# Kernel optimization log

Hardware: AMD Instinct MI355X
Metric: run time of the kernel (lower is better)

## Reference

```python
import math
import jax, jax.numpy as jnp
import numpy as np

B, S, D, H, REL_V = 2, 2048, 1024, 16, 64
HD = D // H
EPS = 1e-5


def _layernorm(x, w, b):
    # torch-style: std with Bessel correction (unbiased), divide by (std + eps)
    u = x.mean(-1, keepdims=True)
    xc = x - u
    s = jnp.sqrt((xc * xc).sum(-1, keepdims=True) / (x.shape[-1] - 1))
    return w * (xc / (s + EPS)) + b


def _gelu(x):
    return 0.5 * x * (1 + jnp.tanh(math.sqrt(2 / math.pi) * (x + 0.044715 * x ** 3)))


def setup_inputs() -> dict:
    key = jax.random.key(0)
    ks = jax.random.split(key, 6)
    wscale = 0.02
    return {
        "x": jax.random.normal(ks[0], (B, S, D), jnp.float32),
        "rel": jax.random.randint(ks[1], (B, S, S), 0, REL_V, jnp.int32),
        "ln1_w": jnp.ones((D,), jnp.float32),
        "ln1_b": jnp.zeros((D,), jnp.float32),
        "Wqkv": jax.random.normal(ks[2], (D, 3 * D), jnp.float32) * wscale,
        "bqkv": jnp.zeros((3 * D,), jnp.float32),
        "Wo": jax.random.normal(ks[3], (D, D), jnp.float32) * wscale,
        "bo": jnp.zeros((D,), jnp.float32),
        "rel_emb": jax.random.normal(ks[4], (REL_V, H), jnp.float32) * wscale,
        "ln2_w": jnp.ones((D,), jnp.float32),
        "ln2_b": jnp.zeros((D,), jnp.float32),
        "Wfc": jax.random.normal(ks[5], (D, 4 * D), jnp.float32) * wscale,
        "bfc": jnp.zeros((4 * D,), jnp.float32),
        "Wp": jax.random.normal(jax.random.fold_in(key, 7), (4 * D, D), jnp.float32) * wscale,
        "bp": jnp.zeros((D,), jnp.float32),
    }


def reference(x, rel, ln1_w, ln1_b, Wqkv, bqkv, Wo, bo, rel_emb,
              ln2_w, ln2_b, Wfc, bfc, Wp, bp):
    h = _layernorm(x, ln1_w, ln1_b)
    qkv = h @ Wqkv + bqkv  # [B,S,3D]
    q, k, v = jnp.split(qkv, 3, axis=-1)
    q = q.reshape(B, S, H, HD).transpose(0, 2, 1, 3)  # [B,H,S,HD]
    k = k.reshape(B, S, H, HD).transpose(0, 2, 1, 3)
    v = v.reshape(B, S, H, HD).transpose(0, 2, 1, 3)

    w = jnp.einsum('bhqd,bhkd->bhqk', q, k) / math.sqrt(HD)  # scale=True
    mask = jnp.tril(jnp.ones((S, S), w.dtype))  # causal tril buffer
    w = w * mask - 1e10 * (1 - mask)
    # faithful to original: rel bias multiplies masked logits (zeroing masked -1e10)
    relw = rel_emb[rel]                    # [B,S,S,H]
    relw = relw.transpose(0, 3, 1, 2)      # [B,H,S,S]
    w = w * (relw * mask)
    p = jax.nn.softmax(w, axis=-1)
    a = jnp.einsum('bhqk,bhkd->bhqd', p, v)       # [B,H,S,HD]
    a = a.transpose(0, 2, 1, 3).reshape(B, S, D)  # merge heads
    a = a @ Wo + bo

    x = x + a
    m = _gelu(_layernorm(x, ln2_w, ln2_b) @ Wfc + bfc) @ Wp + bp
    return x + m
```

## Files before the change

kernel.cpp:

```cpp
#include <hip/hip_runtime.h>
#include <hip/hip_bf16.h>
#include <math.h>

using bf16 = __hip_bfloat16;
typedef __bf16 bf16x8 __attribute__((ext_vector_type(8)));
typedef float f32x4 __attribute__((ext_vector_type(4)));

#define SEQ 2048
#define DIM 1024
#define NH 16
#define HDIM 64
#define BATCH 2

__device__ __forceinline__ void load_lds16(const bf16* g, bf16* l) {
  __builtin_amdgcn_global_load_lds((__attribute__((address_space(1))) void*)g,
                                   (__attribute__((address_space(3))) void*)l, 16, 0, 0);
}

__global__ __launch_bounds__(256) void transpose_k(const float* __restrict__ in,
                                                   bf16* __restrict__ out, int R, int C) {
  __shared__ float tile[32][33];
  int c0 = blockIdx.x * 32, r0 = blockIdx.y * 32;
  int tx = threadIdx.x, ty = threadIdx.y;
#pragma unroll
  for (int j = 0; j < 4; ++j)
    tile[ty + 8 * j][tx] = in[(size_t)(r0 + ty + 8 * j) * C + c0 + tx];
  __syncthreads();
#pragma unroll
  for (int j = 0; j < 4; ++j)
    out[(size_t)(c0 + ty + 8 * j) * R + r0 + tx] = __float2bfloat16(tile[tx][ty + 8 * j]);
}

__global__ __launch_bounds__(256) void ln_k(const float* __restrict__ x,
                                            const float* __restrict__ w,
                                            const float* __restrict__ bb,
                                            bf16* __restrict__ out) {
  int row = blockIdx.x, tid = threadIdx.x;
  int wid = tid >> 6, lane = tid & 63;
  const float* xr = x + (size_t)row * DIM;
  float v[4];
#pragma unroll
  for (int j = 0; j < 4; ++j) v[j] = xr[tid + 256 * j];
  float s = v[0] + v[1] + v[2] + v[3];
#pragma unroll
  for (int m = 1; m < 64; m <<= 1) s += __shfl_xor(s, m, 64);
  __shared__ float red[8];
  if (lane == 0) red[wid] = s;
  __syncthreads();
  float mean = (red[0] + red[1] + red[2] + red[3]) * (1.f / DIM);
  float q = 0.f;
#pragma unroll
  for (int j = 0; j < 4; ++j) {
    v[j] -= mean;
    q += v[j] * v[j];
  }
#pragma unroll
  for (int m = 1; m < 64; m <<= 1) q += __shfl_xor(q, m, 64);
  if (lane == 0) red[4 + wid] = q;
  __syncthreads();
  float ssq = red[4] + red[5] + red[6] + red[7];
  float sd = sqrtf(ssq / (float)(DIM - 1));
  float inv = 1.f / (sd + 1e-5f);
#pragma unroll
  for (int j = 0; j < 4; ++j) {
    int c = tid + 256 * j;
    float y = w[c] * (v[j] * inv) + bb[c];
    out[(size_t)row * DIM + c] = __float2bfloat16(y);
  }
}

template <int TM>
__global__ __launch_bounds__(256) void gemm_k(
    const bf16* __restrict__ A, const bf16* __restrict__ Bt, const float* __restrict__ bias,
    int M, int N, int K, int mode,
    bf16* __restrict__ o0, bf16* __restrict__ o1, bf16* __restrict__ o2,
    const float* __restrict__ residf, float* __restrict__ x2out, const float* __restrict__ x2in,
    float* __restrict__ outf) {
  constexpr int MT = TM / 32;
  constexpr int ACH = TM / 8;
  __shared__ bf16 As[TM * 64];
  __shared__ bf16 Bs[128 * 64];
  int tid = threadIdx.x;
  int wid = tid >> 6, lane = tid & 63, quad = lane >> 4, l15 = lane & 15;
  int wm = wid >> 1, wn = wid & 1;
  int m0 = blockIdx.y * TM, n0 = blockIdx.x * 128;
  int rsub = lane >> 3;
  int c8 = (lane & 7) ^ rsub;
  f32x4 acc[MT][4] = {};

  for (int k0 = 0; k0 < K; k0 += 64) {
    __syncthreads();
#pragma unroll
    for (int it = 0; it < ACH / 4; ++it) {
      int c = wid * (ACH / 4) + it;
      int row = c * 8 + rsub;
      load_lds16(A + (size_t)(m0 + row) * K + k0 + c8 * 8, &As[c * 512]);
    }
#pragma unroll
    for (int it = 0; it < 4; ++it) {
      int c = wid * 4 + it;
      int row = c * 8 + rsub;
      load_lds16(Bt + (size_t)(n0 + row) * K + k0 + c8 * 8, &Bs[c * 512]);
    }
    __syncthreads();
#pragma unroll
    for (int ks = 0; ks < 2; ++ks) {
      bf16x8 af[MT], bfr[4];
#pragma unroll
      for (int mt = 0; mt < MT; ++mt) {
        int r = wm * (MT * 16) + mt * 16 + l15;
        af[mt] = *(const bf16x8*)&As[r * 64 + ((ks * 4 + quad) ^ (r & 7)) * 8];
      }
#pragma unroll
      for (int nt = 0; nt < 4; ++nt) {
        int r = wn * 64 + nt * 16 + l15;
        bfr[nt] = *(const bf16x8*)&Bs[r * 64 + ((ks * 4 + quad) ^ (r & 7)) * 8];
      }
#pragma unroll
      for (int mt = 0; mt < MT; ++mt)
#pragma unroll
        for (int nt = 0; nt < 4; ++nt)
          acc[mt][nt] =
              __builtin_amdgcn_mfma_f32_16x16x32_bf16(af[mt], bfr[nt], acc[mt][nt], 0, 0, 0);
    }
  }

#pragma unroll
  for (int mt = 0; mt < MT; ++mt) {
#pragma unroll
    for (int nt = 0; nt < 4; ++nt) {
      int col = n0 + wn * 64 + nt * 16 + l15;
      float bv = bias[col];
      int row_base = m0 + wm * (MT * 16) + mt * 16 + quad * 4;
      if (mode == 0) {
        int which = col >> 10, d = col & 1023, hh = d >> 6, dd = d & 63;
        int b = row_base >> 11, s2 = row_base & 2047;
        if (which == 2) {
          unsigned short pk[4];
#pragma unroll
          for (int r = 0; r < 4; ++r)
            pk[r] = __bfloat16_as_ushort(__float2bfloat16(acc[mt][nt][r] + bv));
          *(uint2*)&o2[(((size_t)b * NH + hh) * HDIM + dd) * SEQ + s2] = *(uint2*)pk;
        } else {
          bf16* dst = which == 0 ? o0 : o1;
#pragma unroll
          for (int r = 0; r < 4; ++r)
            dst[(((size_t)b * NH + hh) * SEQ + s2 + r) * HDIM + dd] =
                __float2bfloat16(acc[mt][nt][r] + bv);
        }
      } else {
#pragma unroll
        for (int r = 0; r < 4; ++r) {
          int row = row_base + r;
          float val = acc[mt][nt][r] + bv;
          if (mode == 1) {
            size_t i = (size_t)row * N + col;
            x2out[i] = residf[i] + val;
          } else if (mode == 2) {
            float t = val;
            float g = 0.5f * t * (1.f + tanhf(0.7978845608028654f * (t + 0.044715f * t * t * t)));
            o0[(size_t)row * N + col] = __float2bfloat16(g);
          } else {
            size_t i = (size_t)row * N + col;
            outf[i] = x2in[i] + val;
          }
        }
      }
    }
  }
}

__global__ __launch_bounds__(256) void sufv_k(const bf16* __restrict__ vt,
                                              float* __restrict__ suf) {
  int row = blockIdx.x;
  const bf16* src = vt + (size_t)row * SEQ;
  float* dst = suf + (size_t)row * SEQ;
  int tid = threadIdx.x;
  float v[8];
  float s = 0.f;
#pragma unroll
  for (int j = 0; j < 8; ++j) {
    v[j] = __bfloat162float(src[tid * 8 + j]);
    s += v[j];
  }
  __shared__ float sc[256];
  sc[tid] = s;
  __syncthreads();
  for (int off = 1; off < 256; off <<= 1) {
    float add = (tid + off < 256) ? sc[tid + off] : 0.f;
    __syncthreads();
    sc[tid] += add;
    __syncthreads();
  }
  float run = (tid < 255) ? sc[tid + 1] : 0.f;
#pragma unroll
  for (int j = 7; j >= 0; --j) {
    dst[tid * 8 + j] = run;
    run += v[j];
  }
}

__global__ __launch_bounds__(256) void attn_k(const bf16* __restrict__ q,
                                              const bf16* __restrict__ k,
                                              const bf16* __restrict__ v,
                                              const int* __restrict__ rel,
                                              const float* __restrict__ rel_emb,
                                              const float* __restrict__ suf,
                                              bf16* __restrict__ out) {
  int h = blockIdx.x;
  int qt = (SEQ / 64 - 1) - blockIdx.y;
  int b = blockIdx.z;
  int tid = threadIdx.x;
  int wid = tid >> 6, lane = tid & 63, quad = lane >> 4, l15 = lane & 15;

  __shared__ bf16 Qs[64 * 64];
  __shared__ bf16 Ks[64 * 64];
  __shared__ bf16 Vt[64 * 64];
  __shared__ __align__(16) char PM[17408];
  bf16(*Ps)[72] = (bf16(*)[72])PM;
  float(*SufLds)[68] = (float(*)[68])PM;

  const size_t bh = (size_t)b * NH + h;
  const bf16* qb = q + (bh * SEQ + (size_t)qt * 64) * HDIM;
  const bf16* kb0 = k + bh * SEQ * HDIM;
  const bf16* vt0 = v + bh * (size_t)HDIM * SEQ;

  float rv = 0.125f * rel_emb[lane * NH + h];

  int rsub = lane >> 3, c8 = lane & 7;
#pragma unroll
  for (int it = 0; it < 2; ++it) {
    int c = wid * 2 + it;
    int row = c * 8 + rsub;
    load_lds16(qb + (size_t)row * HDIM + c8 * 8, &Qs[c * 512]);
  }
  __syncthreads();

  bf16x8 aq[2];
#pragma unroll
  for (int ks = 0; ks < 2; ++ks)
    aq[ks] = *(const bf16x8*)&Qs[(wid * 16 + l15) * 64 + (ks * 4 + quad) * 8];

  const int q_base = qt * 64 + wid * 16 + quad * 4;
  float l_part[4] = {0.f, 0.f, 0.f, 0.f};
  f32x4 o_acc[4] = {};

  const int* relq = rel + (size_t)b * SEQ * SEQ + (size_t)qt * 64 * SEQ;
  const int* rp[4];
#pragma unroll
  for (int r = 0; r < 4; ++r) rp[r] = relq + (size_t)(wid * 16 + quad * 4 + r) * SEQ;

  for (int kt = 0; kt <= qt; ++kt) {
    __syncthreads();
#pragma unroll
    for (int it = 0; it < 2; ++it) {
      int c = wid * 2 + it;
      int row = c * 8 + rsub;
      load_lds16(kb0 + (size_t)(kt * 64 + row) * HDIM + c8 * 8, &Ks[c * 512]);
      load_lds16(vt0 + (size_t)row * SEQ + kt * 64 + c8 * 8, &Vt[c * 512]);
    }
    int ridx[4][4];
#pragma unroll
    for (int nt = 0; nt < 4; ++nt)
#pragma unroll
      for (int r = 0; r < 4; ++r) ridx[nt][r] = rp[r][kt * 64 + nt * 16 + l15];
    __syncthreads();

    f32x4 sacc[4] = {};
#pragma unroll
    for (int ks = 0; ks < 2; ++ks) {
#pragma unroll
      for (int nt = 0; nt < 4; ++nt) {
        bf16x8 bfr = *(const bf16x8*)&Ks[(nt * 16 + l15) * 64 + (ks * 4 + quad) * 8];
        sacc[nt] = __builtin_amdgcn_mfma_f32_16x16x32_bf16(aq[ks], bfr, sacc[nt], 0, 0, 0);
      }
    }

#pragma unroll
    for (int nt = 0; nt < 4; ++nt) {
#pragma unroll
      for (int r = 0; r < 4; ++r) {
        float m = __shfl(rv, ridx[nt][r], 64);
        float p = __expf(sacc[nt][r] * m);
        if (kt == qt) {
          int k_abs = kt * 64 + nt * 16 + l15;
          if (k_abs > q_base + r) p = 0.f;
        }
        l_part[r] += p;
        Ps[wid * 16 + quad * 4 + r][nt * 16 + l15] = __float2bfloat16(p);
      }
    }

#pragma unroll
    for (int ks = 0; ks < 2; ++ks) {
      bf16x8 af = *(const bf16x8*)&Ps[wid * 16 + l15][ks * 32 + quad * 8];
#pragma unroll
      for (int nt = 0; nt < 4; ++nt) {
        bf16x8 bfr = *(const bf16x8*)&Vt[(nt * 16 + l15) * 64 + (ks * 4 + quad) * 8];
        o_acc[nt] = __builtin_amdgcn_mfma_f32_16x16x32_bf16(af, bfr, o_acc[nt], 0, 0, 0);
      }
    }
  }

#pragma unroll
  for (int r = 0; r < 4; ++r)
#pragma unroll
    for (int m = 1; m < 16; m <<= 1) l_part[r] += __shfl_xor(l_part[r], m, 64);

  __syncthreads();
  const float* sufb = suf + bh * (size_t)HDIM * SEQ + (size_t)qt * 64;
#pragma unroll
  for (int p = 0; p < 4; ++p) {
    int idx = p * 256 + tid;
    int d = idx >> 4, qq = idx & 15;
    *(float4*)&SufLds[d][qq * 4] = *(const float4*)(sufb + (size_t)d * SEQ + qq * 4);
  }
  __syncthreads();

#pragma unroll
  for (int nt = 0; nt < 4; ++nt) {
    int d = nt * 16 + l15;
#pragma unroll
    for (int r = 0; r < 4; ++r) {
      int row = q_base + r;
      int cnt = (SEQ - 1) - row;
      float l = l_part[r] + (float)cnt;
      int q_local = wid * 16 + quad * 4 + r;
      float ov = (o_acc[nt][r] + SufLds[d][q_local]) / l;
      out[((size_t)b * SEQ + row) * DIM + h * HDIM + d] = __float2bfloat16(ov);
    }
  }
}

extern "C" void kernel_launch(void* const* d_in, const int* in_sizes, int n_in,
                              void* d_out, int out_size, void* d_ws, size_t ws_size,
                              hipStream_t stream) {
  const float* x = (const float*)d_in[0];
  const int* rel = (const int*)d_in[1];
  const float* ln1w = (const float*)d_in[2];
  const float* ln1b = (const float*)d_in[3];
  const float* Wqkv = (const float*)d_in[4];
  const float* bqkv = (const float*)d_in[5];
  const float* Wo = (const float*)d_in[6];
  const float* bo = (const float*)d_in[7];
  const float* rel_emb = (const float*)d_in[8];
  const float* ln2w = (const float*)d_in[9];
  const float* ln2b = (const float*)d_in[10];
  const float* Wfc = (const float*)d_in[11];
  const float* bfc = (const float*)d_in[12];
  const float* Wp = (const float*)d_in[13];
  const float* bp = (const float*)d_in[14];
  float* outp = (float*)d_out;

  char* ws = (char*)d_ws;
  const size_t MB = 1u << 20;
  bf16* h = (bf16*)(ws + 0);
  bf16* qb = (bf16*)(ws + 8 * MB);
  bf16* kb = (bf16*)(ws + 16 * MB);
  bf16* vb = (bf16*)(ws + 24 * MB);
  float* x2 = (float*)(ws + 32 * MB);
  float* suf = (float*)(ws + 32 * MB);
  bf16* fcb = (bf16*)(ws + 48 * MB);
  bf16* wqkvT = (bf16*)(ws + 48 * MB);
  bf16* woT = (bf16*)(ws + 54 * MB);
  bf16* wfcT = (bf16*)(ws + 16 * MB);
  bf16* wpT = (bf16*)(ws + 24 * MB);

  dim3 tb(32, 8);
  transpose_k<<<dim3(3072 / 32, 1024 / 32), tb, 0, stream>>>(Wqkv, wqkvT, 1024, 3072);
  transpose_k<<<dim3(1024 / 32, 1024 / 32), tb, 0, stream>>>(Wo, woT, 1024, 1024);

  ln_k<<<BATCH * SEQ, 256, 0, stream>>>(x, ln1w, ln1b, h);

  gemm_k<128><<<dim3(3072 / 128, 4096 / 128), 256, 0, stream>>>(
      h, wqkvT, bqkv, BATCH * SEQ, 3072, 1024, 0, qb, kb, vb, nullptr, nullptr, nullptr,
      nullptr);

  sufv_k<<<BATCH * NH * HDIM, 256, 0, stream>>>(vb, suf);

  attn_k<<<dim3(NH, SEQ / 64, BATCH), 256, 0, stream>>>(qb, kb, vb, rel, rel_emb, suf, h);

  gemm_k<64><<<dim3(1024 / 128, 4096 / 64), 256, 0, stream>>>(
      h, woT, bo, BATCH * SEQ, 1024, 1024, 1, nullptr, nullptr, nullptr, x, x2, nullptr,
      nullptr);

  transpose_k<<<dim3(4096 / 32, 1024 / 32), tb, 0, stream>>>(Wfc, wfcT, 1024, 4096);
  transpose_k<<<dim3(1024 / 32, 4096 / 32), tb, 0, stream>>>(Wp, wpT, 4096, 1024);

  ln_k<<<BATCH * SEQ, 256, 0, stream>>>(x2, ln2w, ln2b, qb);

  gemm_k<128><<<dim3(4096 / 128, 4096 / 128), 256, 0, stream>>>(
      qb, wfcT, bfc, BATCH * SEQ, 4096, 1024, 2, fcb, nullptr, nullptr, nullptr, nullptr,
      nullptr, nullptr);

  gemm_k<64><<<dim3(1024 / 128, 4096 / 64), 256, 0, stream>>>(
      fcb, wpT, bp, BATCH * SEQ, 1024, 4096, 3, nullptr, nullptr, nullptr, nullptr, nullptr, x2,
      outp);
}
```

Measured before the change: 450.4 us.

## Double-buffer attention K/V tiles with swizzled LDS and exp-based GELU

The attention kernel now keeps two LDS buffers for K and V. It prefetches the next key tile and its relative-position indices while computing on the current one, which removes one barrier per iteration and hides global load latency. LDS chunks are XOR-swizzled by row on both the write and the read side to cut bank conflicts in the MFMA fragment reads. GELU is rewritten with the equivalent t/(1+exp(-2u)) form using the fast `__expf` in place of `tanhf`. The cost is more shared memory per block, which may lower occupancy, and slightly different rounding in GELU.

```diff
diff --git a/kernel.cpp b/kernel.cpp
--- a/kernel.cpp
+++ b/kernel.cpp
@@ -158,7 +158,8 @@
             x2out[i] = residf[i] + val;
           } else if (mode == 2) {
             float t = val;
-            float g = 0.5f * t * (1.f + tanhf(0.7978845608028654f * (t + 0.044715f * t * t * t)));
+            float u = 0.7978845608028654f * (t + 0.044715f * t * t * t);
+            float g = t / (1.f + __expf(-2.f * u));
             o0[(size_t)row * N + col] = __float2bfloat16(g);
           } else {
             size_t i = (size_t)row * N + col;
@@ -213,12 +214,12 @@
   int tid = threadIdx.x;
   int wid = tid >> 6, lane = tid & 63, quad = lane >> 4, l15 = lane & 15;
 
-  __shared__ bf16 Qs[64 * 64];
-  __shared__ bf16 Ks[64 * 64];
-  __shared__ bf16 Vt[64 * 64];
-  __shared__ __align__(16) char PM[17408];
-  bf16(*Ps)[72] = (bf16(*)[72])PM;
-  float(*SufLds)[68] = (float(*)[68])PM;
+  __shared__ __align__(16) char SM[50176];
+  bf16* Qs = (bf16*)SM;
+  bf16* Kb = (bf16*)(SM + 8192);
+  bf16* Vb = (bf16*)(SM + 8192 + 16384);
+  bf16(*Ps)[72] = (bf16(*)[72])(SM + 40960);
+  float(*SufLds)[68] = (float(*)[68])(SM + 8192);
 
   const size_t bh = (size_t)b * NH + h;
   const bf16* qb = q + (bh * SEQ + (size_t)qt * 64) * HDIM;
@@ -227,51 +228,69 @@
 
   float rv = 0.125f * rel_emb[lane * NH + h];
 
-  int rsub = lane >> 3, c8 = lane & 7;
+  int rsub = lane >> 3;
+  int c8 = (lane & 7) ^ rsub;
+
 #pragma unroll
   for (int it = 0; it < 2; ++it) {
     int c = wid * 2 + it;
     int row = c * 8 + rsub;
     load_lds16(qb + (size_t)row * HDIM + c8 * 8, &Qs[c * 512]);
-  }
+    load_lds16(kb0 + (size_t)row * HDIM + c8 * 8, &Kb[c * 512]);
+    load_lds16(vt0 + (size_t)row * SEQ + c8 * 8, &Vb[c * 512]);
+  }
+
+  const int* relq = rel + (size_t)b * SEQ * SEQ + (size_t)qt * 64 * SEQ;
+  const int* rp[4];
+#pragma unroll
+  for (int r = 0; r < 4; ++r) rp[r] = relq + (size_t)(wid * 16 + quad * 4 + r) * SEQ;
+
+  int ridx[4][4];
+#pragma unroll
+  for (int nt = 0; nt < 4; ++nt)
+#pragma unroll
+    for (int r = 0; r < 4; ++r) ridx[nt][r] = rp[r][nt * 16 + l15];
+
   __syncthreads();
 
   bf16x8 aq[2];
 #pragma unroll
   for (int ks = 0; ks < 2; ++ks)
-    aq[ks] = *(const bf16x8*)&Qs[(wid * 16 + l15) * 64 + (ks * 4 + quad) * 8];
+    aq[ks] = *(const bf16x8*)&Qs[(wid * 16 + l15) * 64 + ((ks * 4 + quad) ^ (l15 & 7)) * 8];
 
   const int q_base = qt * 64 + wid * 16 + quad * 4;
   float l_part[4] = {0.f, 0.f, 0.f, 0.f};
   f32x4 o_acc[4] = {};
 
-  const int* relq = rel + (size_t)b * SEQ * SEQ + (size_t)qt * 64 * SEQ;
-  const int* rp[4];
-#pragma unroll
-  for (int r = 0; r < 4; ++r) rp[r] = relq + (size_t)(wid * 16 + quad * 4 + r) * SEQ;
-
   for (int kt = 0; kt <= qt; ++kt) {
-    __syncthreads();
-#pragma unroll
-    for (int it = 0; it < 2; ++it) {
-      int c = wid * 2 + it;
-      int row = c * 8 + rsub;
-      load_lds16(kb0 + (size_t)(kt * 64 + row) * HDIM + c8 * 8, &Ks[c * 512]);
-      load_lds16(vt0 + (size_t)row * SEQ + kt * 64 + c8 * 8, &Vt[c * 512]);
-    }
-    int ridx[4][4];
-#pragma unroll
-    for (int nt = 0; nt < 4; ++nt)
-#pragma unroll
-      for (int r = 0; r < 4; ++r) ridx[nt][r] = rp[r][kt * 64 + nt * 16 + l15];
-    __syncthreads();
+    int cur = kt & 1;
+
+    int ridx2[4][4];
+    if (kt < qt) {
+      bf16* Kd = Kb + (cur ^ 1) * 4096;
+      bf16* Vd = Vb + (cur ^ 1) * 4096;
+#pragma unroll
+      for (int it = 0; it < 2; ++it) {
+        int c = wid * 2 + it;
+        int row = c * 8 + rsub;
+        load_lds16(kb0 + (size_t)((kt + 1) * 64 + row) * HDIM + c8 * 8, &Kd[c * 512]);
+        load_lds16(vt0 + (size_t)row * SEQ + (kt + 1) * 64 + c8 * 8, &Vd[c * 512]);
+      }
+#pragma unroll
+      for (int nt = 0; nt < 4; ++nt)
+#pragma unroll
+        for (int r = 0; r < 4; ++r) ridx2[nt][r] = rp[r][(kt + 1) * 64 + nt * 16 + l15];
+    }
+
+    const bf16* Ksb = Kb + cur * 4096;
+    const bf16* Vtb = Vb + cur * 4096;
 
     f32x4 sacc[4] = {};
 #pragma unroll
     for (int ks = 0; ks < 2; ++ks) {
 #pragma unroll
       for (int nt = 0; nt < 4; ++nt) {
-        bf16x8 bfr = *(const bf16x8*)&Ks[(nt * 16 + l15) * 64 + (ks * 4 + quad) * 8];
+        bf16x8 bfr = *(const bf16x8*)&Ksb[(nt * 16 + l15) * 64 + ((ks * 4 + quad) ^ (l15 & 7)) * 8];
         sacc[nt] = __builtin_amdgcn_mfma_f32_16x16x32_bf16(aq[ks], bfr, sacc[nt], 0, 0, 0);
       }
     }
@@ -296,10 +315,19 @@
       bf16x8 af = *(const bf16x8*)&Ps[wid * 16 + l15][ks * 32 + quad * 8];
 #pragma unroll
       for (int nt = 0; nt < 4; ++nt) {
-        bf16x8 bfr = *(const bf16x8*)&Vt[(nt * 16 + l15) * 64 + (ks * 4 + quad) * 8];
+        bf16x8 bfr = *(const bf16x8*)&Vtb[(nt * 16 + l15) * 64 + ((ks * 4 + quad) ^ (l15 & 7)) * 8];
         o_acc[nt] = __builtin_amdgcn_mfma_f32_16x16x32_bf16(af, bfr, o_acc[nt], 0, 0, 0);
       }
     }
+
+    __syncthreads();
+
+    if (kt < qt) {
+#pragma unroll
+      for (int nt = 0; nt < 4; ++nt)
+#pragma unroll
+        for (int r = 0; r < 4; ++r) ridx[nt][r] = ridx2[nt][r];
+    }
   }
 
 #pragma unroll
@@ -307,7 +335,6 @@
 #pragma unroll
     for (int m = 1; m < 16; m <<= 1) l_part[r] += __shfl_xor(l_part[r], m, 64);
 
-  __syncthreads();
   const float* sufb = suf + bh * (size_t)HDIM * SEQ + (size_t)qt * 64;
 #pragma unroll
   for (int p = 0; p < 4; ++p) {
```

Result: faster. 437.3 us (-2.9%).
